# Kernel optimization log

Measured on AMD Instinct MI355X. Metric: run time of the kernel, lower is better.

Reference implementation:

```python
import jax, jax.numpy as jnp
import numpy as np

B, T, C, H = 4, 2048, 1024, 16
D = C // H
SCALE = float(np.sqrt(C / H))  # quadf_scale = sqrt(D) = 8.0


def setup_inputs() -> dict:
    key = jax.random.key(0)
    k1, k2, k3 = jax.random.split(key, 3)
    x = jax.random.normal(k1, (B, T, C), dtype=jnp.float32)
    # torch Linear(C, 3C): y = x @ W.T; we store the transposed weight [C, 3C]
    W_attn = jax.random.normal(k2, (C, 3 * C), dtype=jnp.float32) * 0.02
    W_proj = jax.random.normal(k3, (C, C), dtype=jnp.float32) * 0.02
    return {"x": x, "W_attn": W_attn, "W_proj": W_proj}


def reference(x, W_attn, W_proj):
    # QKV projection
    qkv = x @ W_attn                      # [B, T, 3C]
    q, k, v = jnp.split(qkv, 3, axis=-1)  # each [B, T, C]

    def heads(t):  # [B, T, C] -> [B, H, T, D]
        return t.reshape(B, T, H, D).transpose(0, 2, 1, 3)

    q, k, v = heads(q), heads(k), heads(v)

    # scaled dot-product scores with causal mask
    scores = jnp.einsum("bhtd,bhsd->bhts", q, k) / SCALE  # [B, H, T, T]
    causal = jnp.tril(jnp.ones((T, T), dtype=bool))
    scores = jnp.where(causal, scores, -jnp.inf)
    attn = jax.nn.softmax(scores, axis=-1)
    # dropout = 0.0 (eval mode), so omitted

    y = jnp.einsum("bhts,bhsd->bhtd", attn, v)            # [B, H, T, D]
    y = y.transpose(0, 2, 1, 3).reshape(B, T, C)
    return y @ W_proj
```

## Files before the change

### kernel.cpp

```cpp
#include <hip/hip_runtime.h>
#include <hip/hip_bf16.h>

#define B_ 4
#define T_ 2048
#define C_ 1024
#define H_ 16
#define D_ 64
#define C3 3072

typedef __bf16 bf16x8 __attribute__((ext_vector_type(8)));
typedef __bf16 bf16x4 __attribute__((ext_vector_type(4)));
typedef float f32x4 __attribute__((ext_vector_type(4)));
typedef float f32x16 __attribute__((ext_vector_type(16)));
typedef unsigned u32x4 __attribute__((ext_vector_type(4)));

#define SCALE_LOG2E 0.1803368801111244f

__device__ __forceinline__ void gload_lds16(const void* g, void* lds) {
  __builtin_amdgcn_global_load_lds((const __attribute__((address_space(1))) void*)g,
                                   (__attribute__((address_space(3))) void*)lds, 16, 0, 0);
}

__device__ __forceinline__ int swz128(int row, int chunk) {
  return row * 128 + ((chunk ^ (row & 7)) << 4);
}

__device__ __forceinline__ unsigned cvt_pk_bf16(float a, float b) {
  unsigned r;
  asm("v_cvt_pk_bf16_f32 %0, %1, %2" : "=v"(r) : "v"(a), "v"(b));
  return r;
}

__device__ __forceinline__ void pl32swap(unsigned& x, unsigned& y) {
  asm volatile("v_permlane32_swap_b32 %0, %1" : "+v"(x), "+v"(y));
}

__global__ void cast_x_kernel(const float* __restrict__ in, __bf16* __restrict__ out, int n4) {
  int i = blockIdx.x * blockDim.x + threadIdx.x;
  if (i >= n4) return;
  float4 v = ((const float4*)in)[i];
  bf16x4 o;
  o.x = (__bf16)v.x; o.y = (__bf16)v.y; o.z = (__bf16)v.z; o.w = (__bf16)v.w;
  ((bf16x4*)out)[i] = o;
}

__global__ void transpose_cast_kernel(const float* __restrict__ in, __bf16* __restrict__ out,
                                      int K, int N) {
  __shared__ float tile[32][33];
  int kb = blockIdx.y * 32, nb = blockIdx.x * 32;
  int tx = threadIdx.x, ty = threadIdx.y;
#pragma unroll
  for (int i = 0; i < 4; i++) {
    int r = ty + i * 8;
    tile[r][tx] = in[(size_t)(kb + r) * N + nb + tx];
  }
  __syncthreads();
#pragma unroll
  for (int i = 0; i < 4; i++) {
    int r = ty + i * 8;
    out[(size_t)(nb + r) * K + kb + tx] = (__bf16)tile[tx][r];
  }
}

__global__ void transpose_v_kernel(const __bf16* __restrict__ qkv, __bf16* __restrict__ vT) {
  __shared__ __bf16 tile[32][33];
  int b = blockIdx.z;
  int t0 = blockIdx.x * 32, hv0 = blockIdx.y * 32;
  int tx = threadIdx.x, ty = threadIdx.y;
  const __bf16* src = qkv + (size_t)b * T_ * C3 + 2 * C_;
#pragma unroll
  for (int i = 0; i < 4; i++) {
    int r = ty + i * 8;
    tile[r][tx] = src[(size_t)(t0 + r) * C3 + hv0 + tx];
  }
  __syncthreads();
#pragma unroll
  for (int i = 0; i < 4; i++) {
    int r = ty + i * 8;
    vT[((size_t)b * 1024 + hv0 + r) * T_ + t0 + tx] = tile[tx][r];
  }
}

template <bool OUTF32>
__global__ __launch_bounds__(256) void gemm_bt_kernel(const __bf16* __restrict__ A,
                                                      const __bf16* __restrict__ Bt,
                                                      __bf16* __restrict__ Cb,
                                                      float* __restrict__ Cf,
                                                      int M, int N, int K) {
  __shared__ char ldsbuf[2 * 128 * 128];
  char* ldsA = ldsbuf;
  char* ldsB = ldsbuf + 128 * 128;
  int tid = threadIdx.x, w = tid >> 6, l = tid & 63;
  int gx = gridDim.x;
  int nwg = gx * gridDim.y;
  int orig = blockIdx.y * gx + blockIdx.x;
  int cpx = nwg >> 3;
  int swz = (orig & 7) * cpx + (orig >> 3);
  int bx = swz % gx, by = swz / gx;
  int m0 = by * 128, n0 = bx * 128;
  int wr = w >> 1, wc = w & 1;
  int lr = l & 15, lhi = l >> 4;
  f32x4 acc[4][4];
#pragma unroll
  for (int m = 0; m < 4; m++)
#pragma unroll
    for (int n = 0; n < 4; n++) acc[m][n] = (f32x4){0.f, 0.f, 0.f, 0.f};

  int nK = K >> 6;
  for (int kt = 0; kt < nK; kt++) {
    int k0 = kt << 6;
    __syncthreads();
#pragma unroll
    for (int jj = 0; jj < 4; jj++) {
      int q = w * 4 + jj;
      int row = q * 8 + (l >> 3);
      int cg = (l & 7) ^ ((l >> 3) & 7);
      gload_lds16(A + (size_t)(m0 + row) * K + k0 + cg * 8, ldsA + q * 1024);
      gload_lds16(Bt + (size_t)(n0 + row) * K + k0 + cg * 8, ldsB + q * 1024);
    }
    __syncthreads();
    bf16x8 af[4][2], bfr[4][2];
#pragma unroll
    for (int m = 0; m < 4; m++) {
      int r = wr * 64 + m * 16 + lr;
#pragma unroll
      for (int kc = 0; kc < 2; kc++)
        af[m][kc] = *(const bf16x8*)(ldsA + swz128(r, kc * 4 + lhi));
    }
#pragma unroll
    for (int n = 0; n < 4; n++) {
      int r = wc * 64 + n * 16 + lr;
#pragma unroll
      for (int kc = 0; kc < 2; kc++)
        bfr[n][kc] = *(const bf16x8*)(ldsB + swz128(r, kc * 4 + lhi));
    }
#pragma unroll
    for (int kc = 0; kc < 2; kc++)
#pragma unroll
      for (int m = 0; m < 4; m++)
#pragma unroll
        for (int n = 0; n < 4; n++)
          acc[m][n] =
              __builtin_amdgcn_mfma_f32_16x16x32_bf16(af[m][kc], bfr[n][kc], acc[m][n], 0, 0, 0);
  }

#pragma unroll
  for (int m = 0; m < 4; m++)
#pragma unroll
    for (int n = 0; n < 4; n++)
#pragma unroll
      for (int i = 0; i < 4; i++) {
        int rg = m0 + wr * 64 + m * 16 + lhi * 4 + i;
        int cg = n0 + wc * 64 + n * 16 + lr;
        if (OUTF32)
          Cf[(size_t)rg * N + cg] = acc[m][n][i];
        else
          Cb[(size_t)rg * N + cg] = (__bf16)acc[m][n][i];
      }
}

__global__ __launch_bounds__(256) void attn_kernel(const __bf16* __restrict__ qkv,
                                                   const __bf16* __restrict__ vT,
                                                   __bf16* __restrict__ y) {
  __shared__ __align__(16) char lds[2][16384];
  int tid = threadIdx.x, w = tid >> 6, l = tid & 63;

  int g = blockIdx.x >> 6, bh = blockIdx.x & 63;
  int q2 = g >> 2;
  int qb = (q2 & 1) ? ((q2 == 1) ? g + 4 : g - 12) : (15 - g);
  int b = bh >> 4, h = bh & 15;
  size_t base = (size_t)b * T_ * C3;
  int lq = l & 31, hi = l >> 5;
  int qrow = qb * 128 + w * 32 + lq;
  int q0w = qb * 128 + w * 32;

  int lrow = l >> 3;
  int cg = (l & 7) ^ (lrow & 7);
  const __bf16* kptr = qkv + base + (size_t)(w * 16 + lrow) * C3 + C_ + h * D_ + cg * 8;
  const __bf16* vptr = vT + ((size_t)bh * D_ + w * 16 + lrow) * T_ + cg * 8;

  bf16x8 qf[4];
  {
    const __bf16* qp = qkv + base + (size_t)qrow * C3 + h * D_;
#pragma unroll
    for (int c = 0; c < 4; c++) qf[c] = *(const bf16x8*)(qp + c * 16 + hi * 8);
  }

  f32x16 o[2];
#pragma unroll
  for (int d = 0; d < 2; d++)
#pragma unroll
    for (int i = 0; i < 16; i++) o[d][i] = 0.f;
  float mrun = -__builtin_inff(), lrun = 0.f;

  int nt = 2 * qb + 2;

  {
    char* kb = &lds[0][0];
    char* vb = &lds[0][8192];
    gload_lds16(kptr, kb + w * 2048);
    gload_lds16(kptr + 8 * C3, kb + w * 2048 + 1024);
    gload_lds16(vptr, vb + w * 2048);
    gload_lds16(vptr + 8 * T_, vb + w * 2048 + 1024);
  }

  for (int kt = 0; kt < nt; kt++) {
    int buf = kt & 1;
    __syncthreads();
    if (kt + 1 < nt) {
      char* kb = &lds[buf ^ 1][0];
      char* vb = &lds[buf ^ 1][8192];
      const __bf16* kp = kptr + (size_t)(kt + 1) * 64 * C3;
      const __bf16* vp = vptr + (kt + 1) * 64;
      gload_lds16(kp, kb + w * 2048);
      gload_lds16(kp + 8 * C3, kb + w * 2048 + 1024);
      gload_lds16(vp, vb + w * 2048);
      gload_lds16(vp + 8 * T_, vb + w * 2048 + 1024);
    }
    if (kt * 64 > q0w + 31) continue;
    char* kb = &lds[buf][0];
    char* vb = &lds[buf][8192];

    f32x16 s[2];
#pragma unroll
    for (int b2 = 0; b2 < 2; b2++) {
#pragma unroll
      for (int i = 0; i < 16; i++) s[b2][i] = 0.f;
#pragma unroll
      for (int c = 0; c < 4; c++) {
        bf16x8 kf = *(const bf16x8*)(kb + swz128(b2 * 32 + lq, 2 * c + hi));
        s[b2] = __builtin_amdgcn_mfma_f32_32x32x16_bf16(kf, qf[c], s[b2], 0, 0, 0);
      }
    }

    bool needmask = (kt * 64 + 63) > q0w;
#pragma unroll
    for (int b2 = 0; b2 < 2; b2++)
#pragma unroll
      for (int r = 0; r < 16; r++) {
        float v = s[b2][r] * SCALE_LOG2E;
        if (needmask) {
          int kv = kt * 64 + b2 * 32 + (r & 3) + 8 * (r >> 2) + 4 * hi;
          if (kv > qrow) v = -1e30f;
        }
        s[b2][r] = v;
      }

    float vm[16];
#pragma unroll
    for (int r = 0; r < 16; r++) vm[r] = fmaxf(s[0][r], s[1][r]);
#pragma unroll
    for (int st = 8; st >= 1; st >>= 1)
#pragma unroll
      for (int r = 0; r < st; r++) vm[r] = fmaxf(vm[r], vm[r + st]);
    float tmax = fmaxf(vm[0], __shfl_xor(vm[0], 32));

    if (!__all(tmax - mrun <= 8.0f)) {
      float mnew = fmaxf(mrun, tmax);
      float al = __builtin_amdgcn_exp2f(mrun - mnew);
      mrun = mnew;
      lrun *= al;
#pragma unroll
      for (int d = 0; d < 2; d++)
#pragma unroll
        for (int i = 0; i < 16; i++) o[d][i] *= al;
    }

#pragma unroll
    for (int b2 = 0; b2 < 2; b2++)
#pragma unroll
      for (int r = 0; r < 16; r++) s[b2][r] = __builtin_amdgcn_exp2f(s[b2][r] - mrun);

    float vs[16];
#pragma unroll
    for (int r = 0; r < 16; r++) vs[r] = s[0][r] + s[1][r];
#pragma unroll
    for (int st = 8; st >= 1; st >>= 1)
#pragma unroll
      for (int r = 0; r < st; r++) vs[r] += vs[r + st];
    lrun += vs[0] + __shfl_xor(vs[0], 32);

    bf16x8 pa[4];
#pragma unroll
    for (int b2 = 0; b2 < 2; b2++) {
      unsigned wg[4][2];
#pragma unroll
      for (int gg = 0; gg < 4; gg++) {
        wg[gg][0] = cvt_pk_bf16(s[b2][4 * gg + 0], s[b2][4 * gg + 1]);
        wg[gg][1] = cvt_pk_bf16(s[b2][4 * gg + 2], s[b2][4 * gg + 3]);
      }
#pragma unroll
      for (int cp = 0; cp < 2; cp++) {
        unsigned x0 = wg[2 * cp][0], x1 = wg[2 * cp][1];
        unsigned y0 = wg[2 * cp + 1][0], y1 = wg[2 * cp + 1][1];
        pl32swap(x0, y0);
        pl32swap(x1, y1);
        union { u32x4 u; bf16x8 hh; } uu;
        uu.u = (u32x4){x0, x1, y0, y1};
        pa[b2 * 2 + cp] = uu.hh;
      }
    }

#pragma unroll
    for (int db = 0; db < 2; db++)
#pragma unroll
      for (int c = 0; c < 4; c++) {
        bf16x8 vf = *(const bf16x8*)(vb + swz128(db * 32 + lq, 2 * c + hi));
        o[db] = __builtin_amdgcn_mfma_f32_32x32x16_bf16(vf, pa[c], o[db], 0, 0, 0);
      }
  }

  float inv = 1.f / lrun;
  __bf16* yp = y + (size_t)(b * T_ + qrow) * C_ + h * D_;
#pragma unroll
  for (int db = 0; db < 2; db++)
#pragma unroll
    for (int rr = 0; rr < 4; rr++) {
      bf16x4 ov;
#pragma unroll
      for (int i = 0; i < 4; i++) ov[i] = (__bf16)(o[db][rr * 4 + i] * inv);
      *(bf16x4*)(yp + db * 32 + rr * 8 + hi * 4) = ov;
    }
}

extern "C" void kernel_launch(void* const* d_in, const int* in_sizes, int n_in,
                              void* d_out, int out_size, void* d_ws, size_t ws_size,
                              hipStream_t stream) {
  const float* x = (const float*)d_in[0];
  const float* Wa = (const float*)d_in[1];
  const float* Wp = (const float*)d_in[2];
  float* out = (float*)d_out;
  char* ws = (char*)d_ws;

  __bf16* xb  = (__bf16*)(ws);
  __bf16* yb  = (__bf16*)(ws);
  __bf16* wat = (__bf16*)(ws + 16777216);
  __bf16* wpt = (__bf16*)(ws + 23068672);
  __bf16* qkv = (__bf16*)(ws + 25165824);
  __bf16* vT  = (__bf16*)(ws + 75497472);

  cast_x_kernel<<<8192, 256, 0, stream>>>(x, xb, (B_ * T_ * C_) / 4);
  transpose_cast_kernel<<<dim3(C3 / 32, C_ / 32), dim3(32, 8), 0, stream>>>(Wa, wat, C_, C3);
  transpose_cast_kernel<<<dim3(C_ / 32, C_ / 32), dim3(32, 8), 0, stream>>>(Wp, wpt, C_, C_);

  gemm_bt_kernel<false><<<dim3(C3 / 128, (B_ * T_) / 128), 256, 0, stream>>>(
      xb, wat, qkv, nullptr, B_ * T_, C3, C_);

  transpose_v_kernel<<<dim3(T_ / 32, C_ / 32, B_), dim3(32, 8), 0, stream>>>(qkv, vT);

  attn_kernel<<<dim3(1024), 256, 0, stream>>>(qkv, vT, yb);

  gemm_bt_kernel<true><<<dim3(C_ / 128, (B_ * T_) / 128), 256, 0, stream>>>(
      yb, wpt, nullptr, out, B_ * T_, C_, C_);
}
```

Before: 177.9 us.

## Fuse V transpose and Q scaling into QKV GEMM epilogue; tune softmax reductions

The QKV GEMM epilogue now writes the V columns directly in transposed layout into vT, which removes the separate transpose_v kernel and its extra round trip through global memory. The same epilogue pre-multiplies Q by scale*log2e, so the attention loop no longer multiplies each score. Inside the attention loop, the row max uses v_max3, the row sum uses packed f32 adds, and the QK and PV MFMA blocks are wrapped in s_setprio raises. Rounding Q to bf16 after scaling shifts numerics slightly, and the V epilogue uses narrow strided stores that may coalesce poorly.

```diff
diff --git a/kernel.cpp b/kernel.cpp
--- a/kernel.cpp
+++ b/kernel.cpp
@@ -10,6 +10,7 @@
 
 typedef __bf16 bf16x8 __attribute__((ext_vector_type(8)));
 typedef __bf16 bf16x4 __attribute__((ext_vector_type(4)));
+typedef float f32x2 __attribute__((ext_vector_type(2)));
 typedef float f32x4 __attribute__((ext_vector_type(4)));
 typedef float f32x16 __attribute__((ext_vector_type(16)));
 typedef unsigned u32x4 __attribute__((ext_vector_type(4)));
@@ -33,6 +34,18 @@
 
 __device__ __forceinline__ void pl32swap(unsigned& x, unsigned& y) {
   asm volatile("v_permlane32_swap_b32 %0, %1" : "+v"(x), "+v"(y));
+}
+
+__device__ __forceinline__ float fmax3(float a, float b, float c) {
+  float d;
+  asm("v_max3_f32 %0, %1, %2, %3" : "=v"(d) : "v"(a), "v"(b), "v"(c));
+  return d;
+}
+
+__device__ __forceinline__ f32x2 pk_add(f32x2 a, f32x2 b) {
+  f32x2 d;
+  asm("v_pk_add_f32 %0, %1, %2" : "=v"(d) : "v"(a), "v"(b));
+  return d;
 }
 
 __global__ void cast_x_kernel(const float* __restrict__ in, __bf16* __restrict__ out, int n4) {
@@ -62,30 +75,12 @@
   }
 }
 
-__global__ void transpose_v_kernel(const __bf16* __restrict__ qkv, __bf16* __restrict__ vT) {
-  __shared__ __bf16 tile[32][33];
-  int b = blockIdx.z;
-  int t0 = blockIdx.x * 32, hv0 = blockIdx.y * 32;
-  int tx = threadIdx.x, ty = threadIdx.y;
-  const __bf16* src = qkv + (size_t)b * T_ * C3 + 2 * C_;
-#pragma unroll
-  for (int i = 0; i < 4; i++) {
-    int r = ty + i * 8;
-    tile[r][tx] = src[(size_t)(t0 + r) * C3 + hv0 + tx];
-  }
-  __syncthreads();
-#pragma unroll
-  for (int i = 0; i < 4; i++) {
-    int r = ty + i * 8;
-    vT[((size_t)b * 1024 + hv0 + r) * T_ + t0 + tx] = tile[tx][r];
-  }
-}
-
-template <bool OUTF32>
+template <int MODE>
 __global__ __launch_bounds__(256) void gemm_bt_kernel(const __bf16* __restrict__ A,
                                                       const __bf16* __restrict__ Bt,
                                                       __bf16* __restrict__ Cb,
                                                       float* __restrict__ Cf,
+                                                      __bf16* __restrict__ vT,
                                                       int M, int N, int K) {
   __shared__ char ldsbuf[2 * 128 * 128];
   char* ldsA = ldsbuf;
@@ -144,6 +139,25 @@
               __builtin_amdgcn_mfma_f32_16x16x32_bf16(af[m][kc], bfr[n][kc], acc[m][n], 0, 0, 0);
   }
 
+  if (MODE == 2 && n0 >= 2048) {
+    int bb = m0 >> 11;
+    int tb = (m0 & 2047) + wr * 64 + lhi * 4;
+#pragma unroll
+    for (int n = 0; n < 4; n++) {
+      int vcol = (n0 - 2048) + wc * 64 + n * 16 + lr;
+      __bf16* vp = vT + ((size_t)bb * 1024 + vcol) * T_;
+#pragma unroll
+      for (int m = 0; m < 4; m++) {
+        bf16x4 pv;
+#pragma unroll
+        for (int i = 0; i < 4; i++) pv[i] = (__bf16)acc[m][n][i];
+        *(bf16x4*)(vp + tb + m * 16) = pv;
+      }
+    }
+    return;
+  }
+
+  float oscale = (MODE == 2 && n0 < 1024) ? SCALE_LOG2E : 1.0f;
 #pragma unroll
   for (int m = 0; m < 4; m++)
 #pragma unroll
@@ -152,10 +166,10 @@
       for (int i = 0; i < 4; i++) {
         int rg = m0 + wr * 64 + m * 16 + lhi * 4 + i;
         int cg = n0 + wc * 64 + n * 16 + lr;
-        if (OUTF32)
+        if (MODE == 1)
           Cf[(size_t)rg * N + cg] = acc[m][n][i];
         else
-          Cb[(size_t)rg * N + cg] = (__bf16)acc[m][n][i];
+          Cb[(size_t)rg * N + cg] = (__bf16)(acc[m][n][i] * oscale);
       }
 }
 
@@ -186,11 +200,11 @@
     for (int c = 0; c < 4; c++) qf[c] = *(const bf16x8*)(qp + c * 16 + hi * 8);
   }
 
+  f32x16 zacc;
+#pragma unroll
+  for (int i = 0; i < 16; i++) zacc[i] = 0.f;
   f32x16 o[2];
-#pragma unroll
-  for (int d = 0; d < 2; d++)
-#pragma unroll
-    for (int i = 0; i < 16; i++) o[d][i] = 0.f;
+  o[0] = zacc; o[1] = zacc;
   float mrun = -__builtin_inff(), lrun = 0.f;
 
   int nt = 2 * qb + 2;
@@ -222,63 +236,75 @@
     char* vb = &lds[buf][8192];
 
     f32x16 s[2];
+    __builtin_amdgcn_s_setprio(1);
 #pragma unroll
     for (int b2 = 0; b2 < 2; b2++) {
-#pragma unroll
-      for (int i = 0; i < 16; i++) s[b2][i] = 0.f;
-#pragma unroll
-      for (int c = 0; c < 4; c++) {
+      bf16x8 kf0 = *(const bf16x8*)(kb + swz128(b2 * 32 + lq, hi));
+      s[b2] = __builtin_amdgcn_mfma_f32_32x32x16_bf16(kf0, qf[0], zacc, 0, 0, 0);
+#pragma unroll
+      for (int c = 1; c < 4; c++) {
         bf16x8 kf = *(const bf16x8*)(kb + swz128(b2 * 32 + lq, 2 * c + hi));
         s[b2] = __builtin_amdgcn_mfma_f32_32x32x16_bf16(kf, qf[c], s[b2], 0, 0, 0);
       }
     }
-
-    bool needmask = (kt * 64 + 63) > q0w;
+    __builtin_amdgcn_s_setprio(0);
+
+    if (kt * 64 + 63 > q0w) {
+#pragma unroll
+      for (int b2 = 0; b2 < 2; b2++)
+#pragma unroll
+        for (int r = 0; r < 16; r++) {
+          int kv = kt * 64 + b2 * 32 + ((r & 3) + 8 * (r >> 2)) + 4 * hi;
+          if (kv > qrow) s[b2][r] = -1e30f;
+        }
+    }
+
+    {
+      auto xi = [&](int i) -> float { return i < 16 ? s[0][i] : s[1][i - 16]; };
+      float t10[11];
+#pragma unroll
+      for (int g3 = 0; g3 < 10; g3++) t10[g3] = fmax3(xi(3 * g3), xi(3 * g3 + 1), xi(3 * g3 + 2));
+      t10[10] = fmaxf(xi(30), xi(31));
+      float u0 = fmax3(t10[0], t10[1], t10[2]);
+      float u1 = fmax3(t10[3], t10[4], t10[5]);
+      float u2 = fmax3(t10[6], t10[7], t10[8]);
+      float u3 = fmaxf(t10[9], t10[10]);
+      float tl = fmaxf(fmax3(u0, u1, u2), u3);
+      float tmax = fmaxf(tl, __shfl_xor(tl, 32));
+
+      if (!__all(tmax - mrun <= 8.0f)) {
+        float mnew = fmaxf(mrun, tmax);
+        float al = __builtin_amdgcn_exp2f(mrun - mnew);
+        mrun = mnew;
+        lrun *= al;
+#pragma unroll
+        for (int d = 0; d < 2; d++)
+#pragma unroll
+          for (int i = 0; i < 16; i++) o[d][i] *= al;
+      }
+    }
+
 #pragma unroll
     for (int b2 = 0; b2 < 2; b2++)
 #pragma unroll
-      for (int r = 0; r < 16; r++) {
-        float v = s[b2][r] * SCALE_LOG2E;
-        if (needmask) {
-          int kv = kt * 64 + b2 * 32 + (r & 3) + 8 * (r >> 2) + 4 * hi;
-          if (kv > qrow) v = -1e30f;
-        }
-        s[b2][r] = v;
-      }
-
-    float vm[16];
-#pragma unroll
-    for (int r = 0; r < 16; r++) vm[r] = fmaxf(s[0][r], s[1][r]);
-#pragma unroll
-    for (int st = 8; st >= 1; st >>= 1)
-#pragma unroll
-      for (int r = 0; r < st; r++) vm[r] = fmaxf(vm[r], vm[r + st]);
-    float tmax = fmaxf(vm[0], __shfl_xor(vm[0], 32));
-
-    if (!__all(tmax - mrun <= 8.0f)) {
-      float mnew = fmaxf(mrun, tmax);
-      float al = __builtin_amdgcn_exp2f(mrun - mnew);
-      mrun = mnew;
-      lrun *= al;
-#pragma unroll
-      for (int d = 0; d < 2; d++)
-#pragma unroll
-        for (int i = 0; i < 16; i++) o[d][i] *= al;
-    }
-
-#pragma unroll
-    for (int b2 = 0; b2 < 2; b2++)
-#pragma unroll
       for (int r = 0; r < 16; r++) s[b2][r] = __builtin_amdgcn_exp2f(s[b2][r] - mrun);
 
-    float vs[16];
-#pragma unroll
-    for (int r = 0; r < 16; r++) vs[r] = s[0][r] + s[1][r];
-#pragma unroll
-    for (int st = 8; st >= 1; st >>= 1)
-#pragma unroll
-      for (int r = 0; r < st; r++) vs[r] += vs[r + st];
-    lrun += vs[0] + __shfl_xor(vs[0], 32);
+    {
+      f32x2 p8[8];
+#pragma unroll
+      for (int g3 = 0; g3 < 8; g3++) {
+        f32x2 a = {s[0][2 * g3], s[0][2 * g3 + 1]};
+        f32x2 b2v = {s[1][2 * g3], s[1][2 * g3 + 1]};
+        p8[g3] = pk_add(a, b2v);
+      }
+#pragma unroll
+      for (int g3 = 0; g3 < 4; g3++) p8[g3] = pk_add(p8[g3], p8[g3 + 4]);
+      p8[0] = pk_add(p8[0], p8[2]);
+      p8[1] = pk_add(p8[1], p8[3]);
+      p8[0] = pk_add(p8[0], p8[1]);
+      float rs = p8[0][0] + p8[0][1];
+      lrun += rs + __shfl_xor(rs, 32);
+    }
 
     bf16x8 pa[4];
 #pragma unroll
@@ -301,6 +327,7 @@
       }
     }
 
+    __builtin_amdgcn_s_setprio(1);
 #pragma unroll
     for (int db = 0; db < 2; db++)
 #pragma unroll
@@ -308,6 +335,7 @@
         bf16x8 vf = *(const bf16x8*)(vb + swz128(db * 32 + lq, 2 * c + hi));
         o[db] = __builtin_amdgcn_mfma_f32_32x32x16_bf16(vf, pa[c], o[db], 0, 0, 0);
       }
+    __builtin_amdgcn_s_setprio(0);
   }
 
   float inv = 1.f / lrun;
@@ -343,13 +371,11 @@
   transpose_cast_kernel<<<dim3(C3 / 32, C_ / 32), dim3(32, 8), 0, stream>>>(Wa, wat, C_, C3);
   transpose_cast_kernel<<<dim3(C_ / 32, C_ / 32), dim3(32, 8), 0, stream>>>(Wp, wpt, C_, C_);
 
-  gemm_bt_kernel<false><<<dim3(C3 / 128, (B_ * T_) / 128), 256, 0, stream>>>(
-      xb, wat, qkv, nullptr, B_ * T_, C3, C_);
-
-  transpose_v_kernel<<<dim3(T_ / 32, C_ / 32, B_), dim3(32, 8), 0, stream>>>(qkv, vT);
+  gemm_bt_kernel<2><<<dim3(C3 / 128, (B_ * T_) / 128), 256, 0, stream>>>(
+      xb, wat, qkv, nullptr, vT, B_ * T_, C3, C_);
 
   attn_kernel<<<dim3(1024), 256, 0, stream>>>(qkv, vT, yb);
 
-  gemm_bt_kernel<true><<<dim3(C_ / 128, (B_ * T_) / 128), 256, 0, stream>>>(
-      yb, wpt, nullptr, out, B_ * T_, C_, C_);
-}
+  gemm_bt_kernel<1><<<dim3(C_ / 128, (B_ * T_) / 128), 256, 0, stream>>>(
+      yb, wpt, nullptr, out, nullptr, B_ * T_, C_, C_);
+}
```

Result: faster. 164.9 us (-7.3%).
